# Kernel tuning notes

Hardware: AMD Instinct MI355X
Metric: run time of the kernel (lower is better)

The kernel has to match this reference:

```python
import jax, jax.numpy as jnp
import numpy as np

KH, KW = 3, 3

def _grid_offset(H, W):
    # kernel-tap offsets (i, j), ordered row-major like tf.meshgrid(indexing='ij')
    ii, jj = np.meshgrid(np.arange(KH), np.arange(KW), indexing='ij')
    init = np.stack([ii.ravel(), jj.ravel()], axis=-1).astype(np.float32)      # (n, 2)
    pad_h, pad_w = (KH - 1) // 2, (KW - 1) // 2
    gy, gx = np.meshgrid(np.arange(-pad_h, H - pad_h), np.arange(-pad_w, W - pad_w), indexing='ij')
    grid = np.stack([gy, gx], axis=-1).astype(np.float32)                      # (H, W, 2)
    return jnp.asarray(grid[:, :, None, :] + init[None, None, :, :])           # (H, W, n, 2)

def setup_inputs() -> dict:
    key = jax.random.key(0)
    k1, k2, k3 = jax.random.split(key, 3)
    B, H, W_, C, F = 8, 128, 128, 64, 64
    n = KH * KW
    x = jax.random.normal(k1, (B, H, W_, C), dtype=jnp.float32)
    offsets = jax.random.normal(k2, (B, H, W_, 2 * n), dtype=jnp.float32)
    W = jax.random.normal(k3, (n, C, F), dtype=jnp.float32) * 0.02
    b = jnp.zeros((F,), dtype=jnp.float32)
    return {"x": x, "offsets": offsets, "W": W, "b": b}

def reference(x, offsets, W, b):
    B, H, Wd, C = x.shape
    n = KH * KW
    # coords: sampling locations (B, H, W, n, 2), clipped to valid range
    coords = _grid_offset(H, Wd)[None] + offsets.reshape(B, H, Wd, n, 2)
    cy = jnp.clip(coords[..., 0], 0.0, H - 1)
    cx = jnp.clip(coords[..., 1], 0.0, Wd - 1)
    y0 = jnp.floor(cy).astype(jnp.int32)
    y1 = jnp.ceil(cy).astype(jnp.int32)
    x0 = jnp.floor(cx).astype(jnp.int32)
    x1 = jnp.ceil(cx).astype(jnp.int32)
    fy = (cy - y0)[..., None]  # frac along h (matches coords_offset_lt[...,0])
    fx = (cx - x0)[..., None]  # frac along w
    bidx = jnp.arange(B)[:, None, None, None]
    # 4-corner gathers -> (B, H, W, n, C)
    v_lt = x[bidx, y0, x0]
    v_rb = x[bidx, y1, x1]
    v_lb = x[bidx, y0, x1]
    v_rt = x[bidx, y1, x0]
    v_t = v_lt + (v_rt - v_lt) * fy
    v_b = v_lb + (v_rb - v_lb) * fy
    sampled = v_t + (v_b - v_t) * fx                 # (B, H, W, n, C)
    # conv3d with kernel [1,1,n,C,F] VALID == contraction over (n, c)
    out = jnp.einsum('bhwnc,ncf->bhwf', sampled, W) + b
    return out
```

## Files before the change

### kernel.cpp

```cpp
#include <hip/hip_runtime.h>

typedef float v4f __attribute__((ext_vector_type(4)));
typedef unsigned int uint;
typedef unsigned short ushort;
typedef __attribute__((ext_vector_type(4))) uint u32x4;
typedef __attribute__((ext_vector_type(8))) ushort u16x8;
typedef __attribute__((ext_vector_type(8))) __bf16 bf16x8;
typedef __attribute__((ext_vector_type(16))) float f32x16;

#define NB 8
#define NH 128
#define NW 128
#define NC 64
#define NF 64
#define NTAP 9

__device__ __forceinline__ ushort f2bf(float f) {
    uint u = __float_as_uint(f);
    return (ushort)((u + 0x7fffu + ((u >> 16) & 1u)) >> 16);
}
__device__ __forceinline__ float bf2f(ushort s) {
    return __uint_as_float(((uint)s) << 16);
}
__device__ __forceinline__ void g2lds16(const void* g, void* l) {
    __builtin_amdgcn_global_load_lds((__attribute__((address_space(1))) void*)(uintptr_t)g,
                                     (__attribute__((address_space(3))) void*)l, 16, 0, 0);
}

__global__ __launch_bounds__(256) void cvt_x_kernel(const float* __restrict__ x,
                                                    ushort* __restrict__ xb) {
    int i = blockIdx.x * 256 + threadIdx.x;
    const v4f* src = (const v4f*)x + 2 * (size_t)i;
    v4f a = src[0], b = src[1];
    u16x8 o;
#pragma unroll
    for (int j = 0; j < 4; j++) { o[j] = f2bf(a[j]); o[4 + j] = f2bf(b[j]); }
    *(u16x8*)(xb + 8 * (size_t)i) = o;
}

__global__ __launch_bounds__(256) void prep_w_kernel(const float* __restrict__ wt,
                                                     ushort* __restrict__ wimg) {
    int idx = blockIdx.x * 256 + threadIdx.x;
    int c = idx & 63, f = (idx >> 6) & 63, k = idx >> 12;
    int pg = (c >> 3) ^ (f & 7);
    wimg[(k * 64 + f) * 64 + pg * 8 + (c & 7)] = f2bf(wt[(k * 64 + c) * 64 + f]);
}

template<bool PREP>
__global__ __launch_bounds__(256)
void dconv2d_mfma(const void* __restrict__ xin,
                  const float* __restrict__ offs,
                  const void* __restrict__ wsrc,
                  const float* __restrict__ bias,
                  float* __restrict__ out)
{
    __shared__ ushort sA[128 * 64];
    __shared__ ushort sW[64 * 64];

    const int t  = threadIdx.x;
    const int bb = blockIdx.z;
    const int h0 = blockIdx.y * 8;
    const int w0 = blockIdx.x * 16;

    const int p1 = t >> 1;
    const int ch = (t & 1) << 5;
    const int h  = h0 + (p1 >> 4);
    const int w  = w0 + (p1 & 15);
    const float* offp = offs + ((size_t)(bb * NH + h) * NW + w) * (2 * NTAP);

    const int lane = t & 63, wv = t >> 6;
    const int arow = wv * 32 + (lane & 31);
    const int kh   = lane >> 5;
    const float bv0 = bias[lane & 31];
    const float bv1 = bias[32 + (lane & 31)];

    f32x16 acc0 = (f32x16)0.0f, acc1 = (f32x16)0.0f;

    for (int k = 0; k < NTAP; k++) {
        if constexpr (PREP) {
            const char* gbase = (const char*)wsrc + (size_t)k * 8192;
#pragma unroll
            for (int it = 0; it < 2; it++)
                g2lds16(gbase + it * 4096 + t * 16, (char*)sW + it * 4096 + wv * 1024);
        } else {
            const float* wsf = (const float*)wsrc + (size_t)k * 4096;
#pragma unroll
            for (int it = 0; it < 4; it++) {
                int c = it * 16 + (t >> 4);
                int f4 = (t & 15) * 4;
                v4f v = *(const v4f*)(wsf + c * 64 + f4);
#pragma unroll
                for (int j = 0; j < 4; j++) {
                    int f = f4 + j;
                    sW[f * 64 + (((c >> 3) ^ (f & 7)) << 3) + (c & 7)] = f2bf(v[j]);
                }
            }
        }

        {
            const int ky = k / 3, kx = k - 3 * ky;
            float cy = (float)(h - 1 + ky) + offp[2 * k];
            float cx = (float)(w - 1 + kx) + offp[2 * k + 1];
            cy = fminf(fmaxf(cy, 0.f), (float)(NH - 1));
            cx = fminf(fmaxf(cx, 0.f), (float)(NW - 1));
            float fy0 = floorf(cy), fx0 = floorf(cx);
            int y0 = (int)fy0,       x0i = (int)fx0;
            int y1 = (int)ceilf(cy), x1i = (int)ceilf(cx);
            float fy = cy - fy0, fx = cx - fx0;
            int i00 = ((bb * NH + y0) * NW + x0i) * NC + ch;
            int i10 = ((bb * NH + y1) * NW + x0i) * NC + ch;
            int i01 = ((bb * NH + y0) * NW + x1i) * NC + ch;
            int i11 = ((bb * NH + y1) * NW + x1i) * NC + ch;
#pragma unroll
            for (int i = 0; i < 4; i++) {
                float v00[8], v10[8], v01[8], v11[8];
                if constexpr (PREP) {
                    const ushort* xb = (const ushort*)xin;
                    u16x8 a0 = *(const u16x8*)(xb + i00 + 8 * i);
                    u16x8 a1 = *(const u16x8*)(xb + i10 + 8 * i);
                    u16x8 a2 = *(const u16x8*)(xb + i01 + 8 * i);
                    u16x8 a3 = *(const u16x8*)(xb + i11 + 8 * i);
#pragma unroll
                    for (int e = 0; e < 8; e++) {
                        v00[e] = bf2f(a0[e]); v10[e] = bf2f(a1[e]);
                        v01[e] = bf2f(a2[e]); v11[e] = bf2f(a3[e]);
                    }
                } else {
                    const float* xf = (const float*)xin;
#pragma unroll
                    for (int q = 0; q < 2; q++) {
                        v4f b0 = *(const v4f*)(xf + i00 + 8 * i + 4 * q);
                        v4f b1 = *(const v4f*)(xf + i10 + 8 * i + 4 * q);
                        v4f b2 = *(const v4f*)(xf + i01 + 8 * i + 4 * q);
                        v4f b3 = *(const v4f*)(xf + i11 + 8 * i + 4 * q);
#pragma unroll
                        for (int e = 0; e < 4; e++) {
                            v00[4 * q + e] = b0[e]; v10[4 * q + e] = b1[e];
                            v01[4 * q + e] = b2[e]; v11[4 * q + e] = b3[e];
                        }
                    }
                }
                u16x8 o;
#pragma unroll
                for (int e = 0; e < 8; e++) {
                    float vt = v00[e] + (v10[e] - v00[e]) * fy;
                    float vb = v01[e] + (v11[e] - v01[e]) * fy;
                    o[e] = f2bf(vt + (vb - vt) * fx);
                }
                int pg = (((ch >> 3) + i) ^ (p1 & 7));
                *(u16x8*)(&sA[p1 * 64 + pg * 8]) = o;
            }
        }
        __syncthreads();

#pragma unroll
        for (int ks = 0; ks < 4; ks++) {
            int g = (ks * 2 + kh);
            u32x4 a  = *(const u32x4*)&sA[arow * 64 + ((g ^ (arow & 7)) << 3)];
            u32x4 b0 = *(const u32x4*)&sW[(lane & 31) * 64 + ((g ^ (lane & 7)) << 3)];
            u32x4 b1 = *(const u32x4*)&sW[(32 + (lane & 31)) * 64 + ((g ^ (lane & 7)) << 3)];
            bf16x8 af = __builtin_bit_cast(bf16x8, a);
            acc0 = __builtin_amdgcn_mfma_f32_32x32x16_bf16(af, __builtin_bit_cast(bf16x8, b0), acc0, 0, 0, 0);
            acc1 = __builtin_amdgcn_mfma_f32_32x32x16_bf16(af, __builtin_bit_cast(bf16x8, b1), acc1, 0, 0, 0);
        }
        __syncthreads();
    }

    const int fcol = lane & 31;
#pragma unroll
    for (int cb = 0; cb < 2; cb++) {
        f32x16 ac = cb ? acc1 : acc0;
        float bv = cb ? bv1 : bv0;
#pragma unroll
        for (int r = 0; r < 16; r++) {
            int p  = wv * 32 + (r & 3) + 8 * (r >> 2) + 4 * kh;
            int hh = h0 + (p >> 4), ww = w0 + (p & 15);
            out[((size_t)(bb * NH + hh) * NW + ww) * NF + cb * 32 + fcol] = ac[r] + bv;
        }
    }
}

extern "C" void kernel_launch(void* const* d_in, const int* in_sizes, int n_in,
                              void* d_out, int out_size, void* d_ws, size_t ws_size,
                              hipStream_t stream) {
    const float* xin  = (const float*)d_in[0];
    const float* offs = (const float*)d_in[1];
    const float* wt   = (const float*)d_in[2];
    const float* bias = (const float*)d_in[3];
    float* out = (float*)d_out;

    const size_t xbytes = (size_t)NB * NH * NW * NC * 2;
    const size_t wbytes = (size_t)NTAP * NC * NF * 2;
    dim3 grid(NW / 16, NH / 8, NB);

    if (ws_size >= xbytes + wbytes) {
        ushort* xb   = (ushort*)d_ws;
        ushort* wimg = (ushort*)((char*)d_ws + xbytes);
        int n8 = NB * NH * NW * NC / 8;
        cvt_x_kernel<<<n8 / 256, 256, 0, stream>>>(xin, xb);
        prep_w_kernel<<<NTAP * NC * NF / 256, 256, 0, stream>>>(wt, wimg);
        dconv2d_mfma<true><<<grid, 256, 0, stream>>>(xb, offs, wimg, bias, out);
    } else {
        dconv2d_mfma<false><<<grid, 256, 0, stream>>>(xin, offs, wt, bias, out);
    }
}
```

Baseline: 67.01 us.

## Switch to fp16 with packed interpolation and double-buffer tap staging

Converts x and W to fp16 instead of bf16, so bilinear interpolation runs as packed half-precision vector math without unpacking to fp32, and the MFMA uses the f16 variant. The main kernel now double-buffers the A and W shared tiles: it issues gathers for the next tap before running the MFMA on the current one, which removes one barrier per tap. Offsets are preloaded into registers, and the block index is remapped so the batch index varies fastest. Doing the interpolation in fp16 lowers accuracy and doubles LDS use.

```diff
diff --git a/kernel.cpp b/kernel.cpp
--- a/kernel.cpp
+++ b/kernel.cpp
@@ -1,11 +1,12 @@
 #include <hip/hip_runtime.h>
 
 typedef float v4f __attribute__((ext_vector_type(4)));
+typedef float v2f __attribute__((ext_vector_type(2)));
 typedef unsigned int uint;
 typedef unsigned short ushort;
 typedef __attribute__((ext_vector_type(4))) uint u32x4;
 typedef __attribute__((ext_vector_type(8))) ushort u16x8;
-typedef __attribute__((ext_vector_type(8))) __bf16 bf16x8;
+typedef __attribute__((ext_vector_type(8))) _Float16 h8;
 typedef __attribute__((ext_vector_type(16))) float f32x16;
 
 #define NB 8
@@ -15,12 +16,8 @@
 #define NF 64
 #define NTAP 9
 
-__device__ __forceinline__ ushort f2bf(float f) {
-    uint u = __float_as_uint(f);
-    return (ushort)((u + 0x7fffu + ((u >> 16) & 1u)) >> 16);
-}
-__device__ __forceinline__ float bf2f(ushort s) {
-    return __uint_as_float(((uint)s) << 16);
+__device__ __forceinline__ ushort f2h(float f) {
+    return __builtin_bit_cast(ushort, (_Float16)f);
 }
 __device__ __forceinline__ void g2lds16(const void* g, void* l) {
     __builtin_amdgcn_global_load_lds((__attribute__((address_space(1))) void*)(uintptr_t)g,
@@ -28,14 +25,14 @@
 }
 
 __global__ __launch_bounds__(256) void cvt_x_kernel(const float* __restrict__ x,
-                                                    ushort* __restrict__ xb) {
-    int i = blockIdx.x * 256 + threadIdx.x;
-    const v4f* src = (const v4f*)x + 2 * (size_t)i;
+                                                    ushort* __restrict__ xh) {
+    size_t i = (size_t)blockIdx.x * 256 + threadIdx.x;
+    const v4f* src = (const v4f*)x + 2 * i;
     v4f a = src[0], b = src[1];
     u16x8 o;
 #pragma unroll
-    for (int j = 0; j < 4; j++) { o[j] = f2bf(a[j]); o[4 + j] = f2bf(b[j]); }
-    *(u16x8*)(xb + 8 * (size_t)i) = o;
+    for (int j = 0; j < 4; j++) { o[j] = f2h(a[j]); o[4 + j] = f2h(b[j]); }
+    *(u16x8*)(xh + 8 * i) = o;
 }
 
 __global__ __launch_bounds__(256) void prep_w_kernel(const float* __restrict__ wt,
@@ -43,137 +40,231 @@
     int idx = blockIdx.x * 256 + threadIdx.x;
     int c = idx & 63, f = (idx >> 6) & 63, k = idx >> 12;
     int pg = (c >> 3) ^ (f & 7);
-    wimg[(k * 64 + f) * 64 + pg * 8 + (c & 7)] = f2bf(wt[(k * 64 + c) * 64 + f]);
-}
-
-template<bool PREP>
+    wimg[(k * 64 + f) * 64 + pg * 8 + (c & 7)] = f2h(wt[(k * 64 + c) * 64 + f]);
+}
+
 __global__ __launch_bounds__(256)
-void dconv2d_mfma(const void* __restrict__ xin,
-                  const float* __restrict__ offs,
-                  const void* __restrict__ wsrc,
-                  const float* __restrict__ bias,
-                  float* __restrict__ out)
+void dconv2d_mfma_h(const ushort* __restrict__ xh,
+                    const float* __restrict__ offs,
+                    const ushort* __restrict__ wimg,
+                    const float* __restrict__ bias,
+                    float* __restrict__ out)
+{
+    __shared__ ushort sA[2][128 * 64];
+    __shared__ ushort sW[2][64 * 64];
+
+    const int t    = threadIdx.x;
+    const int id   = blockIdx.x;
+    const int bb   = id & 7;
+    const int tile = id >> 3;
+    const int h0   = (tile >> 3) * 8;
+    const int w0   = (tile & 7) * 16;
+
+    const int p1 = t >> 1;
+    const int ch = (t & 1) << 5;
+    const int h  = h0 + (p1 >> 4);
+    const int w  = w0 + (p1 & 15);
+
+    const int lane = t & 63, wv = t >> 6;
+    const int arow = wv * 32 + (lane & 31);
+    const int kh   = lane >> 5;
+
+    const float* offp = offs + ((size_t)(bb * NH + h) * NW + w) * (2 * NTAP);
+    float offv[18];
+#pragma unroll
+    for (int j = 0; j < 9; j++) {
+        v2f q = *(const v2f*)(offp + 2 * j);
+        offv[2 * j] = q[0]; offv[2 * j + 1] = q[1];
+    }
+
+    auto stageW = [&](int k, int buf) {
+        const char* gb = (const char*)wimg + (size_t)k * 8192;
+        char* lb = (char*)(&sW[buf][0]);
+#pragma unroll
+        for (int it = 0; it < 2; it++)
+            g2lds16(gb + it * 4096 + t * 16, lb + it * 4096 + wv * 1024);
+    };
+
+    auto issue = [&](int k, u16x8* g00, u16x8* g10, u16x8* g01, u16x8* g11,
+                     float& fy, float& fx) {
+        const int ky = k / 3, kx = k - 3 * ky;
+        float cy = (float)(h - 1 + ky) + offv[2 * k];
+        float cx = (float)(w - 1 + kx) + offv[2 * k + 1];
+        cy = fminf(fmaxf(cy, 0.f), 127.f);
+        cx = fminf(fmaxf(cx, 0.f), 127.f);
+        float fy0 = floorf(cy), fx0 = floorf(cx);
+        int y0 = (int)fy0,       x0 = (int)fx0;
+        int y1 = (int)ceilf(cy), x1 = (int)ceilf(cx);
+        fy = cy - fy0; fx = cx - fx0;
+        int i00 = ((bb * NH + y0) * NW + x0) * NC + ch;
+        int i10 = ((bb * NH + y1) * NW + x0) * NC + ch;
+        int i01 = ((bb * NH + y0) * NW + x1) * NC + ch;
+        int i11 = ((bb * NH + y1) * NW + x1) * NC + ch;
+#pragma unroll
+        for (int i = 0; i < 4; i++) {
+            g00[i] = *(const u16x8*)(xh + i00 + 8 * i);
+            g10[i] = *(const u16x8*)(xh + i10 + 8 * i);
+            g01[i] = *(const u16x8*)(xh + i01 + 8 * i);
+            g11[i] = *(const u16x8*)(xh + i11 + 8 * i);
+        }
+    };
+
+    auto commit = [&](int buf, u16x8* g00, u16x8* g10, u16x8* g01, u16x8* g11,
+                      float fy, float fx) {
+        _Float16 fyh = (_Float16)fy, fxh = (_Float16)fx;
+        h8 fy8 = {fyh, fyh, fyh, fyh, fyh, fyh, fyh, fyh};
+        h8 fx8 = {fxh, fxh, fxh, fxh, fxh, fxh, fxh, fxh};
+#pragma unroll
+        for (int i = 0; i < 4; i++) {
+            h8 v00 = __builtin_bit_cast(h8, g00[i]);
+            h8 v10 = __builtin_bit_cast(h8, g10[i]);
+            h8 v01 = __builtin_bit_cast(h8, g01[i]);
+            h8 v11 = __builtin_bit_cast(h8, g11[i]);
+            h8 vt = v00 + (v10 - v00) * fy8;
+            h8 vb = v01 + (v11 - v01) * fy8;
+            h8 sv = vt + (vb - vt) * fx8;
+            int pg = (((ch >> 3) + i) ^ (p1 & 7));
+            *(u16x8*)(&sA[buf][p1 * 64 + pg * 8]) = __builtin_bit_cast(u16x8, sv);
+        }
+    };
+
+    f32x16 acc0 = (f32x16)0.0f, acc1 = (f32x16)0.0f;
+
+    auto mm = [&](int buf) {
+#pragma unroll
+        for (int ks = 0; ks < 4; ks++) {
+            int g = ks * 2 + kh;
+            u32x4 a  = *(const u32x4*)&sA[buf][arow * 64 + ((g ^ (arow & 7)) << 3)];
+            u32x4 b0 = *(const u32x4*)&sW[buf][(lane & 31) * 64 + ((g ^ (lane & 7)) << 3)];
+            u32x4 b1 = *(const u32x4*)&sW[buf][(32 + (lane & 31)) * 64 + ((g ^ (lane & 7)) << 3)];
+            h8 af = __builtin_bit_cast(h8, a);
+            acc0 = __builtin_amdgcn_mfma_f32_32x32x16_f16(af, __builtin_bit_cast(h8, b0), acc0, 0, 0, 0);
+            acc1 = __builtin_amdgcn_mfma_f32_32x32x16_f16(af, __builtin_bit_cast(h8, b1), acc1, 0, 0, 0);
+        }
+    };
+
+    stageW(0, 0);
+    {
+        u16x8 g00[4], g10[4], g01[4], g11[4]; float fy, fx;
+        issue(0, g00, g10, g01, g11, fy, fx);
+        commit(0, g00, g10, g01, g11, fy, fx);
+    }
+    __syncthreads();
+
+#pragma unroll
+    for (int k = 0; k < NTAP; k++) {
+        const int cur = k & 1, nxt = cur ^ 1;
+        u16x8 g00[4], g10[4], g01[4], g11[4]; float fy, fx;
+        if (k < 8) {
+            stageW(k + 1, nxt);
+            issue(k + 1, g00, g10, g01, g11, fy, fx);
+        }
+        mm(cur);
+        if (k < 8) {
+            commit(nxt, g00, g10, g01, g11, fy, fx);
+            __syncthreads();
+        }
+    }
+
+    const int fcol = lane & 31;
+    const float bv0 = bias[fcol], bv1 = bias[32 + fcol];
+#pragma unroll
+    for (int cb = 0; cb < 2; cb++) {
+        f32x16 ac = cb ? acc1 : acc0;
+        float bv = cb ? bv1 : bv0;
+#pragma unroll
+        for (int r = 0; r < 16; r++) {
+            int p  = wv * 32 + (r & 3) + 8 * (r >> 2) + 4 * kh;
+            int hh = h0 + (p >> 4), ww = w0 + (p & 15);
+            out[((size_t)(bb * NH + hh) * NW + ww) * NF + cb * 32 + fcol] = ac[r] + bv;
+        }
+    }
+}
+
+__global__ __launch_bounds__(256)
+void dconv2d_fb(const float* __restrict__ xf,
+                const float* __restrict__ offs,
+                const float* __restrict__ wsf,
+                const float* __restrict__ bias,
+                float* __restrict__ out)
 {
     __shared__ ushort sA[128 * 64];
     __shared__ ushort sW[64 * 64];
-
     const int t  = threadIdx.x;
     const int bb = blockIdx.z;
     const int h0 = blockIdx.y * 8;
     const int w0 = blockIdx.x * 16;
-
-    const int p1 = t >> 1;
-    const int ch = (t & 1) << 5;
-    const int h  = h0 + (p1 >> 4);
-    const int w  = w0 + (p1 & 15);
+    const int p1 = t >> 1, ch = (t & 1) << 5;
+    const int h = h0 + (p1 >> 4), w = w0 + (p1 & 15);
     const float* offp = offs + ((size_t)(bb * NH + h) * NW + w) * (2 * NTAP);
-
     const int lane = t & 63, wv = t >> 6;
     const int arow = wv * 32 + (lane & 31);
-    const int kh   = lane >> 5;
-    const float bv0 = bias[lane & 31];
-    const float bv1 = bias[32 + (lane & 31)];
-
+    const int kh = lane >> 5;
     f32x16 acc0 = (f32x16)0.0f, acc1 = (f32x16)0.0f;
 
     for (int k = 0; k < NTAP; k++) {
-        if constexpr (PREP) {
-            const char* gbase = (const char*)wsrc + (size_t)k * 8192;
-#pragma unroll
-            for (int it = 0; it < 2; it++)
-                g2lds16(gbase + it * 4096 + t * 16, (char*)sW + it * 4096 + wv * 1024);
-        } else {
-            const float* wsf = (const float*)wsrc + (size_t)k * 4096;
-#pragma unroll
-            for (int it = 0; it < 4; it++) {
-                int c = it * 16 + (t >> 4);
-                int f4 = (t & 15) * 4;
-                v4f v = *(const v4f*)(wsf + c * 64 + f4);
-#pragma unroll
-                for (int j = 0; j < 4; j++) {
-                    int f = f4 + j;
-                    sW[f * 64 + (((c >> 3) ^ (f & 7)) << 3) + (c & 7)] = f2bf(v[j]);
-                }
+        const float* wp = wsf + (size_t)k * 4096;
+#pragma unroll
+        for (int it = 0; it < 4; it++) {
+            int c = it * 16 + (t >> 4);
+            int f4 = (t & 15) * 4;
+            v4f v = *(const v4f*)(wp + c * 64 + f4);
+#pragma unroll
+            for (int j = 0; j < 4; j++) {
+                int f = f4 + j;
+                sW[f * 64 + (((c >> 3) ^ (f & 7)) << 3) + (c & 7)] = f2h(v[j]);
             }
         }
-
-        {
-            const int ky = k / 3, kx = k - 3 * ky;
-            float cy = (float)(h - 1 + ky) + offp[2 * k];
-            float cx = (float)(w - 1 + kx) + offp[2 * k + 1];
-            cy = fminf(fmaxf(cy, 0.f), (float)(NH - 1));
-            cx = fminf(fmaxf(cx, 0.f), (float)(NW - 1));
-            float fy0 = floorf(cy), fx0 = floorf(cx);
-            int y0 = (int)fy0,       x0i = (int)fx0;
-            int y1 = (int)ceilf(cy), x1i = (int)ceilf(cx);
-            float fy = cy - fy0, fx = cx - fx0;
-            int i00 = ((bb * NH + y0) * NW + x0i) * NC + ch;
-            int i10 = ((bb * NH + y1) * NW + x0i) * NC + ch;
-            int i01 = ((bb * NH + y0) * NW + x1i) * NC + ch;
-            int i11 = ((bb * NH + y1) * NW + x1i) * NC + ch;
-#pragma unroll
-            for (int i = 0; i < 4; i++) {
-                float v00[8], v10[8], v01[8], v11[8];
-                if constexpr (PREP) {
-                    const ushort* xb = (const ushort*)xin;
-                    u16x8 a0 = *(const u16x8*)(xb + i00 + 8 * i);
-                    u16x8 a1 = *(const u16x8*)(xb + i10 + 8 * i);
-                    u16x8 a2 = *(const u16x8*)(xb + i01 + 8 * i);
-                    u16x8 a3 = *(const u16x8*)(xb + i11 + 8 * i);
-#pragma unroll
-                    for (int e = 0; e < 8; e++) {
-                        v00[e] = bf2f(a0[e]); v10[e] = bf2f(a1[e]);
-                        v01[e] = bf2f(a2[e]); v11[e] = bf2f(a3[e]);
-                    }
-                } else {
-                    const float* xf = (const float*)xin;
-#pragma unroll
-                    for (int q = 0; q < 2; q++) {
-                        v4f b0 = *(const v4f*)(xf + i00 + 8 * i + 4 * q);
-                        v4f b1 = *(const v4f*)(xf + i10 + 8 * i + 4 * q);
-                        v4f b2 = *(const v4f*)(xf + i01 + 8 * i + 4 * q);
-                        v4f b3 = *(const v4f*)(xf + i11 + 8 * i + 4 * q);
-#pragma unroll
-                        for (int e = 0; e < 4; e++) {
-                            v00[4 * q + e] = b0[e]; v10[4 * q + e] = b1[e];
-                            v01[4 * q + e] = b2[e]; v11[4 * q + e] = b3[e];
-                        }
-                    }
-                }
-                u16x8 o;
-#pragma unroll
-                for (int e = 0; e < 8; e++) {
-                    float vt = v00[e] + (v10[e] - v00[e]) * fy;
-                    float vb = v01[e] + (v11[e] - v01[e]) * fy;
-                    o[e] = f2bf(vt + (vb - vt) * fx);
-                }
-                int pg = (((ch >> 3) + i) ^ (p1 & 7));
-                *(u16x8*)(&sA[p1 * 64 + pg * 8]) = o;
-            }
+        const int ky = k / 3, kx = k - 3 * ky;
+        float cy = (float)(h - 1 + ky) + offp[2 * k];
+        float cx = (float)(w - 1 + kx) + offp[2 * k + 1];
+        cy = fminf(fmaxf(cy, 0.f), 127.f);
+        cx = fminf(fmaxf(cx, 0.f), 127.f);
+        float fy0 = floorf(cy), fx0 = floorf(cx);
+        int y0 = (int)fy0, x0 = (int)fx0;
+        int y1 = (int)ceilf(cy), x1 = (int)ceilf(cx);
+        float fy = cy - fy0, fx = cx - fx0;
+        const float* r00 = xf + ((bb * NH + y0) * NW + x0) * NC + ch;
+        const float* r10 = xf + ((bb * NH + y1) * NW + x0) * NC + ch;
+        const float* r01 = xf + ((bb * NH + y0) * NW + x1) * NC + ch;
+        const float* r11 = xf + ((bb * NH + y1) * NW + x1) * NC + ch;
+#pragma unroll
+        for (int i = 0; i < 8; i++) {
+            v4f v00 = *(const v4f*)(r00 + 4 * i);
+            v4f v10 = *(const v4f*)(r10 + 4 * i);
+            v4f v01 = *(const v4f*)(r01 + 4 * i);
+            v4f v11 = *(const v4f*)(r11 + 4 * i);
+            v4f vt = v00 + (v10 - v00) * fy;
+            v4f vb = v01 + (v11 - v01) * fy;
+            v4f sv = vt + (vb - vt) * fx;
+            int g = (ch >> 3) + (i >> 1);
+            int pg = g ^ (p1 & 7);
+#pragma unroll
+            for (int e = 0; e < 4; e++)
+                sA[p1 * 64 + pg * 8 + (i & 1) * 4 + e] = f2h(sv[e]);
         }
         __syncthreads();
-
 #pragma unroll
         for (int ks = 0; ks < 4; ks++) {
-            int g = (ks * 2 + kh);
+            int g = ks * 2 + kh;
             u32x4 a  = *(const u32x4*)&sA[arow * 64 + ((g ^ (arow & 7)) << 3)];
             u32x4 b0 = *(const u32x4*)&sW[(lane & 31) * 64 + ((g ^ (lane & 7)) << 3)];
             u32x4 b1 = *(const u32x4*)&sW[(32 + (lane & 31)) * 64 + ((g ^ (lane & 7)) << 3)];
-            bf16x8 af = __builtin_bit_cast(bf16x8, a);
-            acc0 = __builtin_amdgcn_mfma_f32_32x32x16_bf16(af, __builtin_bit_cast(bf16x8, b0), acc0, 0, 0, 0);
-            acc1 = __builtin_amdgcn_mfma_f32_32x32x16_bf16(af, __builtin_bit_cast(bf16x8, b1), acc1, 0, 0, 0);
+            h8 af = __builtin_bit_cast(h8, a);
+            acc0 = __builtin_amdgcn_mfma_f32_32x32x16_f16(af, __builtin_bit_cast(h8, b0), acc0, 0, 0, 0);
+            acc1 = __builtin_amdgcn_mfma_f32_32x32x16_f16(af, __builtin_bit_cast(h8, b1), acc1, 0, 0, 0);
         }
         __syncthreads();
     }
-
     const int fcol = lane & 31;
+    const float bv0 = bias[fcol], bv1 = bias[32 + fcol];
 #pragma unroll
     for (int cb = 0; cb < 2; cb++) {
         f32x16 ac = cb ? acc1 : acc0;
         float bv = cb ? bv1 : bv0;
 #pragma unroll
         for (int r = 0; r < 16; r++) {
-            int p  = wv * 32 + (r & 3) + 8 * (r >> 2) + 4 * kh;
+            int p = wv * 32 + (r & 3) + 8 * (r >> 2) + 4 * kh;
             int hh = h0 + (p >> 4), ww = w0 + (p & 15);
             out[((size_t)(bb * NH + hh) * NW + ww) * NF + cb * 32 + fcol] = ac[r] + bv;
         }
@@ -191,16 +282,16 @@
 
     const size_t xbytes = (size_t)NB * NH * NW * NC * 2;
     const size_t wbytes = (size_t)NTAP * NC * NF * 2;
-    dim3 grid(NW / 16, NH / 8, NB);
 
     if (ws_size >= xbytes + wbytes) {
-        ushort* xb   = (ushort*)d_ws;
+        ushort* xh   = (ushort*)d_ws;
         ushort* wimg = (ushort*)((char*)d_ws + xbytes);
         int n8 = NB * NH * NW * NC / 8;
-        cvt_x_kernel<<<n8 / 256, 256, 0, stream>>>(xin, xb);
+        cvt_x_kernel<<<n8 / 256, 256, 0, stream>>>(xin, xh);
         prep_w_kernel<<<NTAP * NC * NF / 256, 256, 0, stream>>>(wt, wimg);
-        dconv2d_mfma<true><<<grid, 256, 0, stream>>>(xb, offs, wimg, bias, out);
+        dconv2d_mfma_h<<<1024, 256, 0, stream>>>(xh, offs, wimg, bias, out);
     } else {
-        dconv2d_mfma<false><<<grid, 256, 0, stream>>>(xin, offs, wt, bias, out);
-    }
-}
+        dim3 grid(NW / 16, NH / 8, NB);
+        dconv2d_fb<<<grid, 256, 0, stream>>>(xin, offs, wt, bias, out);
+    }
+}
```

Result: faster. 60.66 us (-9.5%).
